# Kernel tuning notes

Measured on AMD Instinct MI355X. Metric: run time of the kernel, lower is better.

The kernel has to match this reference:

```python
import jax, jax.numpy as jnp
import numpy as np

C = 384
K = 13
EPS = 1e-5

def bn(y, g, b, m, v):
    # inference-mode BatchNorm2d over channel dim of NCHW
    scale = (g / jnp.sqrt(v + EPS)).reshape(1, -1, 1, 1)
    shift = (b - m * g / jnp.sqrt(v + EPS)).reshape(1, -1, 1, 1)
    return y * scale + shift

def dwconv(x, w):
    # depthwise KxK conv, SAME padding, w: [C,1,K,K]
    p = w.shape[-1] // 2
    return jax.lax.conv_general_dilated(
        x, w, window_strides=(1, 1), padding=[(p, p), (p, p)],
        dimension_numbers=('NCHW', 'OIHW', 'NCHW'),
        feature_group_count=x.shape[1])

def setup_inputs() -> dict:
    key = jax.random.key(0)
    ks = jax.random.split(key, 16)
    f32 = jnp.float32
    inp = {
        'x':     jax.random.normal(ks[0], (16, C, 56, 56), dtype=f32),
        'pw_w':  jax.random.normal(ks[1], (C, C), dtype=f32) * 0.05,
        'pw_g':  jax.random.uniform(ks[2], (C,), dtype=f32) + 0.5,
        'pw_b':  jax.random.normal(ks[3], (C,), dtype=f32) * 0.1,
        'pw_m':  jax.random.normal(ks[4], (C,), dtype=f32) * 0.1,
        'pw_v':  jax.random.uniform(ks[5], (C,), dtype=f32) + 0.5,
        'dwk_w': jax.random.normal(ks[6], (C, 1, K, K), dtype=f32) * 0.05,
        'dwk_g': jax.random.uniform(ks[7], (C,), dtype=f32) + 0.5,
        'dwk_b': jax.random.normal(ks[8], (C,), dtype=f32) * 0.1,
        'dwk_m': jax.random.normal(ks[9], (C,), dtype=f32) * 0.1,
        'dwk_v': jax.random.uniform(ks[10], (C,), dtype=f32) + 0.5,
        'dw1_w': jax.random.normal(ks[11], (C,), dtype=f32) * 0.5,
        'dw1_g': jax.random.uniform(ks[12], (C,), dtype=f32) + 0.5,
        'dw1_b': jax.random.normal(ks[13], (C,), dtype=f32) * 0.1,
        'dw1_m': jax.random.normal(ks[14], (C,), dtype=f32) * 0.1,
        'dw1_v': jax.random.uniform(ks[15], (C,), dtype=f32) + 0.5,
    }
    return inp

def reference(x, pw_w, pw_g, pw_b, pw_m, pw_v,
              dwk_w, dwk_g, dwk_b, dwk_m, dwk_v,
              dw1_w, dw1_g, dw1_b, dw1_m, dw1_v):
    # pointwise conv (1x1, dense over channels) + BN, residual add
    y = jnp.einsum('bchw,oc->bohw', x, pw_w)
    x_pw = bn(y, pw_g, pw_b, pw_m, pw_v) + x
    # large-kernel depthwise branch
    out = bn(dwconv(x_pw, dwk_w), dwk_g, dwk_b, dwk_m, dwk_v)
    # 1x1 depthwise branch = per-channel scale
    out = out + bn(x_pw * dw1_w.reshape(1, -1, 1, 1), dw1_g, dw1_b, dw1_m, dw1_v)
    return jax.nn.gelu(out, approximate=False)
```

## Files before the change

### kernel.cpp

```cpp
#include <hip/hip_runtime.h>

#define CC 384
#define HW 3136
#define WIDTH 56
#define PLANE_ELEMS (CC*HW)
#define EPS 1e-5f

#define SLOT_U 6272
#define HALF_U 3136

typedef __attribute__((ext_vector_type(8))) short bf16x8;
typedef __attribute__((ext_vector_type(4))) float f32x4;

static __device__ __forceinline__ float bf2f(unsigned short u) {
  union { unsigned int i; float f; } x; x.i = ((unsigned int)u) << 16; return x.f;
}
static __device__ __forceinline__ unsigned short f2bf(float f) {
  union { float f; unsigned int i; } x; x.f = f;
  unsigned int r = x.i + 0x7fffu + ((x.i >> 16) & 1u);
  return (unsigned short)(r >> 16);
}

__global__ __launch_bounds__(256) void pw_gemm_bn_res(
    const float* __restrict__ xin,
    const float* __restrict__ wmat,
    const float* __restrict__ pwg, const float* __restrict__ pwb,
    const float* __restrict__ pwm, const float* __restrict__ pwv,
    unsigned short* __restrict__ xpw)
{
  __shared__ __align__(16) unsigned short Xt[64 * 40];
  __shared__ __align__(16) unsigned short Wt[64 * 40];
  __shared__ float scaleS[64];
  __shared__ float shiftS[64];

  const int tid = threadIdx.x;
  const int j0 = blockIdx.x * 64;
  const int o0 = blockIdx.y * 64;
  const int b  = blockIdx.z;
  const size_t bbase = (size_t)b * PLANE_ELEMS;

  if (tid < 64) {
    int o = o0 + tid;
    float s = pwg[o] * rsqrtf(pwv[o] + EPS);
    scaleS[tid] = s;
    shiftS[tid] = pwb[o] - pwm[o] * s;
  }

  f32x4 acc0 = {0.f,0.f,0.f,0.f}, acc1 = {0.f,0.f,0.f,0.f};
  f32x4 acc2 = {0.f,0.f,0.f,0.f}, acc3 = {0.f,0.f,0.f,0.f};

  const int lane = tid & 63;
  const int wv_  = tid >> 6;
  const int l15  = lane & 15;
  const int q    = lane >> 4;

  const int skk  = tid >> 3;
  const int sjj  = (tid & 7) << 3;
  const int sn   = tid >> 2;
  const int skk0 = (tid & 3) << 3;

  for (int kt = 0; kt < 12; ++kt) {
    const int c0 = kt * 32;
    __syncthreads();
    {
      const float* src = xin + bbase + (size_t)(c0 + skk) * HW + (j0 + sjj);
      float4 p0 = *((const float4*)src);
      float4 p1 = *((const float4*)(src + 4));
      Xt[(sjj + 0) * 40 + skk] = f2bf(p0.x);
      Xt[(sjj + 1) * 40 + skk] = f2bf(p0.y);
      Xt[(sjj + 2) * 40 + skk] = f2bf(p0.z);
      Xt[(sjj + 3) * 40 + skk] = f2bf(p0.w);
      Xt[(sjj + 4) * 40 + skk] = f2bf(p1.x);
      Xt[(sjj + 5) * 40 + skk] = f2bf(p1.y);
      Xt[(sjj + 6) * 40 + skk] = f2bf(p1.z);
      Xt[(sjj + 7) * 40 + skk] = f2bf(p1.w);
    }
    {
      const float* src = wmat + (size_t)(o0 + sn) * CC + (c0 + skk0);
      float4 p0 = *((const float4*)src);
      float4 p1 = *((const float4*)(src + 4));
      ushort4 u0, u1;
      u0.x = f2bf(p0.x); u0.y = f2bf(p0.y); u0.z = f2bf(p0.z); u0.w = f2bf(p0.w);
      u1.x = f2bf(p1.x); u1.y = f2bf(p1.y); u1.z = f2bf(p1.z); u1.w = f2bf(p1.w);
      *((ushort4*)&Wt[sn * 40 + skk0])     = u0;
      *((ushort4*)&Wt[sn * 40 + skk0 + 4]) = u1;
    }
    __syncthreads();

    bf16x8 a  = *((const bf16x8*)&Xt[(wv_ * 16 + l15) * 40 + q * 8]);
    bf16x8 b0 = *((const bf16x8*)&Wt[( 0 + l15) * 40 + q * 8]);
    bf16x8 b1 = *((const bf16x8*)&Wt[(16 + l15) * 40 + q * 8]);
    bf16x8 b2 = *((const bf16x8*)&Wt[(32 + l15) * 40 + q * 8]);
    bf16x8 b3 = *((const bf16x8*)&Wt[(48 + l15) * 40 + q * 8]);
    acc0 = __builtin_amdgcn_mfma_f32_16x16x32_bf16(a, b0, acc0, 0, 0, 0);
    acc1 = __builtin_amdgcn_mfma_f32_16x16x32_bf16(a, b1, acc1, 0, 0, 0);
    acc2 = __builtin_amdgcn_mfma_f32_16x16x32_bf16(a, b2, acc2, 0, 0, 0);
    acc3 = __builtin_amdgcn_mfma_f32_16x16x32_bf16(a, b3, acc3, 0, 0, 0);
  }

  const int j = j0 + wv_ * 16 + q * 4;
  #pragma unroll
  for (int nb = 0; nb < 4; ++nb) {
    f32x4 acc = (nb == 0) ? acc0 : (nb == 1) ? acc1 : (nb == 2) ? acc2 : acc3;
    int oo = nb * 16 + l15;
    int o = o0 + oo;
    float s = scaleS[oo], t = shiftS[oo];
    float4 xr = *((const float4*)(xin + bbase + (size_t)o * HW + j));
    ushort4 w4;
    w4.x = f2bf(acc[0] * s + t + xr.x);
    w4.y = f2bf(acc[1] * s + t + xr.y);
    w4.z = f2bf(acc[2] * s + t + xr.z);
    w4.w = f2bf(acc[3] * s + t + xr.w);
    size_t pidx = (size_t)(b * CC + o) * SLOT_U + HALF_U + j;
    *((ushort4*)(xpw + pidx)) = w4;
  }
}

#define TSTRIDE 88
#define TROWS 76

__global__ __launch_bounds__(256) void dw_conv_mfma(
    float* __restrict__ outf,
    const unsigned short* __restrict__ stash,
    const float* __restrict__ dwkw,
    const float* __restrict__ dkg, const float* __restrict__ dkb,
    const float* __restrict__ dkm, const float* __restrict__ dkv,
    const float* __restrict__ d1w,
    const float* __restrict__ d1g, const float* __restrict__ d1b,
    const float* __restrict__ d1m, const float* __restrict__ d1v)
{
  __shared__ __align__(16) unsigned short tile[TROWS * TSTRIDE];
  __shared__ __align__(16) unsigned short Bt[13 * 16 * 32];

  const int bc = blockIdx.x;
  const int c = bc % CC;
  const size_t plane_u = (size_t)bc * SLOT_U + HALF_U;
  const size_t plane_f = (size_t)bc * HW;
  const int tid = threadIdx.x;

  for (int i = tid; i < TROWS * TSTRIDE; i += 256) {
    int r = i / TSTRIDE, col = i - r * TSTRIDE;
    int gy = r - 6, gx = col - 6;
    unsigned short v = 0;
    if ((unsigned)gy < (unsigned)WIDTH && (unsigned)gx < (unsigned)WIDTH)
      v = stash[plane_u + gy * WIDTH + gx];
    tile[i] = v;
  }
  for (int i = tid; i < 13 * 512; i += 256) {
    int ky = i >> 9, rem = i & 511, n = rem >> 5, k = rem & 31;
    int kx = k - n;
    float wv = ((unsigned)kx < 13u) ? dwkw[c * 169 + ky * 13 + kx] : 0.f;
    Bt[i] = f2bf(wv);
  }

  const float sk = dkg[c] * rsqrtf(dkv[c] + EPS);
  const float tk = dkb[c] - dkm[c] * sk;
  const float s1 = d1g[c] * rsqrtf(d1v[c] + EPS);
  const float a1 = d1w[c] * s1;
  const float t1 = d1b[c] - d1m[c] * s1;
  const float tsum = tk + t1;

  __syncthreads();

  const int lane = tid & 63;
  const int l15  = lane & 15;
  const int q    = lane >> 4;
  const int wid  = tid >> 6;

  bf16x8 bfr[13];
  #pragma unroll
  for (int ky = 0; ky < 13; ++ky)
    bfr[ky] = *((const bf16x8*)&Bt[(ky * 16 + l15) * 32 + q * 8]);

  for (int t = wid; t < 16; t += 4) {
    const int y0 = (t >> 2) * 16, x0 = (t & 3) * 16;
    f32x4 acc = {0.f, 0.f, 0.f, 0.f};
    #pragma unroll
    for (int ky = 0; ky < 13; ++ky) {
      bf16x8 a = *((const bf16x8*)&tile[(y0 + l15 + ky) * TSTRIDE + x0 + q * 8]);
      acc = __builtin_amdgcn_mfma_f32_16x16x32_bf16(a, bfr[ky], acc, 0, 0, 0);
    }
    const int x = x0 + l15;
    if (x < WIDTH) {
      #pragma unroll
      for (int r = 0; r < 4; ++r) {
        const int y = y0 + q * 4 + r;
        if (y < WIDTH) {
          float ctr = bf2f(tile[(y + 6) * TSTRIDE + x + 6]);
          float v = acc[r] * sk + tsum + ctr * a1;
          outf[plane_f + y * WIDTH + x] =
              0.5f * v * (1.f + erff(v * 0.70710678118654752f));
        }
      }
    }
  }
}

extern "C" void kernel_launch(void* const* d_in, const int* in_sizes, int n_in,
                              void* d_out, int out_size, void* d_ws, size_t ws_size,
                              hipStream_t stream) {
  const float* x     = (const float*)d_in[0];
  const float* pw_w  = (const float*)d_in[1];
  const float* pw_g  = (const float*)d_in[2];
  const float* pw_b  = (const float*)d_in[3];
  const float* pw_m  = (const float*)d_in[4];
  const float* pw_v  = (const float*)d_in[5];
  const float* dwk_w = (const float*)d_in[6];
  const float* dwk_g = (const float*)d_in[7];
  const float* dwk_b = (const float*)d_in[8];
  const float* dwk_m = (const float*)d_in[9];
  const float* dwk_v = (const float*)d_in[10];
  const float* dw1_w = (const float*)d_in[11];
  const float* dw1_g = (const float*)d_in[12];
  const float* dw1_b = (const float*)d_in[13];
  const float* dw1_m = (const float*)d_in[14];
  const float* dw1_v = (const float*)d_in[15];
  float* outf = (float*)d_out;
  unsigned short* outu = (unsigned short*)d_out;

  dim3 gridA(HW / 64, CC / 64, 16);
  pw_gemm_bn_res<<<gridA, 256, 0, stream>>>(x, pw_w, pw_g, pw_b, pw_m, pw_v, outu);

  dim3 gridB(16 * CC);
  dw_conv_mfma<<<gridB, 256, 0, stream>>>(outf, outu, dwk_w,
      dwk_g, dwk_b, dwk_m, dwk_v, dw1_w, dw1_g, dw1_b, dw1_m, dw1_v);
}
```

Baseline: 306.6 us.

## Load GEMM operands straight into registers and vectorize depthwise tile fill

The pointwise GEMM kernel no longer stages X and W through LDS with barriers. Each lane loads its MFMA fragments directly from global memory, using strided scalar loads for X and float4 loads for W, and packs them to bf16 with the packed conversion intrinsic. The BN scale and shift are now computed per lane instead of through shared memory. The depthwise kernel fills its halo tile with 16-byte vector loads by shifting the tile origin to an 8-element aligned offset, with the weight band and centre index adjusted to match. The trade is fewer barriers and fewer LDS transposes against uncoalesced strided X loads and redundant W loads across waves.

```diff
diff --git a/kernel.cpp b/kernel.cpp
--- a/kernel.cpp
+++ b/kernel.cpp
@@ -1,4 +1,5 @@
 #include <hip/hip_runtime.h>
+#include <hip/hip_bf16.h>
 
 #define CC 384
 #define HW 3136
@@ -19,6 +20,10 @@
   union { float f; unsigned int i; } x; x.f = f;
   unsigned int r = x.i + 0x7fffu + ((x.i >> 16) & 1u);
   return (unsigned short)(r >> 16);
+}
+static __device__ __forceinline__ unsigned int pkbf(float a, float b) {
+  __hip_bfloat162 h = __float22bfloat162_rn(float2{a, b});
+  union { __hip_bfloat162 h; unsigned int u; } c; c.h = h; return c.u;
 }
 
 __global__ __launch_bounds__(256) void pw_gemm_bn_res(
@@ -28,83 +33,61 @@
     const float* __restrict__ pwm, const float* __restrict__ pwv,
     unsigned short* __restrict__ xpw)
 {
-  __shared__ __align__(16) unsigned short Xt[64 * 40];
-  __shared__ __align__(16) unsigned short Wt[64 * 40];
-  __shared__ float scaleS[64];
-  __shared__ float shiftS[64];
-
   const int tid = threadIdx.x;
   const int j0 = blockIdx.x * 64;
   const int o0 = blockIdx.y * 64;
   const int b  = blockIdx.z;
   const size_t bbase = (size_t)b * PLANE_ELEMS;
 
-  if (tid < 64) {
-    int o = o0 + tid;
-    float s = pwg[o] * rsqrtf(pwv[o] + EPS);
-    scaleS[tid] = s;
-    shiftS[tid] = pwb[o] - pwm[o] * s;
-  }
-
-  f32x4 acc0 = {0.f,0.f,0.f,0.f}, acc1 = {0.f,0.f,0.f,0.f};
-  f32x4 acc2 = {0.f,0.f,0.f,0.f}, acc3 = {0.f,0.f,0.f,0.f};
-
   const int lane = tid & 63;
   const int wv_  = tid >> 6;
   const int l15  = lane & 15;
   const int q    = lane >> 4;
 
-  const int skk  = tid >> 3;
-  const int sjj  = (tid & 7) << 3;
-  const int sn   = tid >> 2;
-  const int skk0 = (tid & 3) << 3;
+  const int jm = j0 + wv_ * 16 + l15;
+  const float* xcol = xin + bbase + jm;
+
+  f32x4 acc0 = {0.f,0.f,0.f,0.f}, acc1 = {0.f,0.f,0.f,0.f};
+  f32x4 acc2 = {0.f,0.f,0.f,0.f}, acc3 = {0.f,0.f,0.f,0.f};
 
   for (int kt = 0; kt < 12; ++kt) {
-    const int c0 = kt * 32;
-    __syncthreads();
-    {
-      const float* src = xin + bbase + (size_t)(c0 + skk) * HW + (j0 + sjj);
-      float4 p0 = *((const float4*)src);
-      float4 p1 = *((const float4*)(src + 4));
-      Xt[(sjj + 0) * 40 + skk] = f2bf(p0.x);
-      Xt[(sjj + 1) * 40 + skk] = f2bf(p0.y);
-      Xt[(sjj + 2) * 40 + skk] = f2bf(p0.z);
-      Xt[(sjj + 3) * 40 + skk] = f2bf(p0.w);
-      Xt[(sjj + 4) * 40 + skk] = f2bf(p1.x);
-      Xt[(sjj + 5) * 40 + skk] = f2bf(p1.y);
-      Xt[(sjj + 6) * 40 + skk] = f2bf(p1.z);
-      Xt[(sjj + 7) * 40 + skk] = f2bf(p1.w);
+    const int c0 = kt * 32 + q * 8;
+    const float* xp = xcol + (size_t)c0 * HW;
+    float a0 = xp[0];
+    float a1 = xp[(size_t)1 * HW];
+    float a2 = xp[(size_t)2 * HW];
+    float a3 = xp[(size_t)3 * HW];
+    float a4 = xp[(size_t)4 * HW];
+    float a5 = xp[(size_t)5 * HW];
+    float a6 = xp[(size_t)6 * HW];
+    float a7 = xp[(size_t)7 * HW];
+    union { bf16x8 v; unsigned int u[4]; } A;
+    A.u[0] = pkbf(a0, a1); A.u[1] = pkbf(a2, a3);
+    A.u[2] = pkbf(a4, a5); A.u[3] = pkbf(a6, a7);
+
+    const float* wrow = wmat + c0 + (size_t)(o0 + l15) * CC;
+    #pragma unroll
+    for (int nb = 0; nb < 4; ++nb) {
+      const float* wp = wrow + (size_t)(nb * 16) * CC;
+      float4 w0 = *((const float4*)wp);
+      float4 w1 = *((const float4*)(wp + 4));
+      union { bf16x8 v; unsigned int u[4]; } B;
+      B.u[0] = pkbf(w0.x, w0.y); B.u[1] = pkbf(w0.z, w0.w);
+      B.u[2] = pkbf(w1.x, w1.y); B.u[3] = pkbf(w1.z, w1.w);
+      if (nb == 0) acc0 = __builtin_amdgcn_mfma_f32_16x16x32_bf16(A.v, B.v, acc0, 0, 0, 0);
+      if (nb == 1) acc1 = __builtin_amdgcn_mfma_f32_16x16x32_bf16(A.v, B.v, acc1, 0, 0, 0);
+      if (nb == 2) acc2 = __builtin_amdgcn_mfma_f32_16x16x32_bf16(A.v, B.v, acc2, 0, 0, 0);
+      if (nb == 3) acc3 = __builtin_amdgcn_mfma_f32_16x16x32_bf16(A.v, B.v, acc3, 0, 0, 0);
     }
-    {
-      const float* src = wmat + (size_t)(o0 + sn) * CC + (c0 + skk0);
-      float4 p0 = *((const float4*)src);
-      float4 p1 = *((const float4*)(src + 4));
-      ushort4 u0, u1;
-      u0.x = f2bf(p0.x); u0.y = f2bf(p0.y); u0.z = f2bf(p0.z); u0.w = f2bf(p0.w);
-      u1.x = f2bf(p1.x); u1.y = f2bf(p1.y); u1.z = f2bf(p1.z); u1.w = f2bf(p1.w);
-      *((ushort4*)&Wt[sn * 40 + skk0])     = u0;
-      *((ushort4*)&Wt[sn * 40 + skk0 + 4]) = u1;
-    }
-    __syncthreads();
-
-    bf16x8 a  = *((const bf16x8*)&Xt[(wv_ * 16 + l15) * 40 + q * 8]);
-    bf16x8 b0 = *((const bf16x8*)&Wt[( 0 + l15) * 40 + q * 8]);
-    bf16x8 b1 = *((const bf16x8*)&Wt[(16 + l15) * 40 + q * 8]);
-    bf16x8 b2 = *((const bf16x8*)&Wt[(32 + l15) * 40 + q * 8]);
-    bf16x8 b3 = *((const bf16x8*)&Wt[(48 + l15) * 40 + q * 8]);
-    acc0 = __builtin_amdgcn_mfma_f32_16x16x32_bf16(a, b0, acc0, 0, 0, 0);
-    acc1 = __builtin_amdgcn_mfma_f32_16x16x32_bf16(a, b1, acc1, 0, 0, 0);
-    acc2 = __builtin_amdgcn_mfma_f32_16x16x32_bf16(a, b2, acc2, 0, 0, 0);
-    acc3 = __builtin_amdgcn_mfma_f32_16x16x32_bf16(a, b3, acc3, 0, 0, 0);
   }
 
   const int j = j0 + wv_ * 16 + q * 4;
   #pragma unroll
   for (int nb = 0; nb < 4; ++nb) {
     f32x4 acc = (nb == 0) ? acc0 : (nb == 1) ? acc1 : (nb == 2) ? acc2 : acc3;
-    int oo = nb * 16 + l15;
-    int o = o0 + oo;
-    float s = scaleS[oo], t = shiftS[oo];
+    int o = o0 + nb * 16 + l15;
+    float s = pwg[o] * rsqrtf(pwv[o] + EPS);
+    float t = pwb[o] - pwm[o] * s;
     float4 xr = *((const float4*)(xin + bbase + (size_t)o * HW + j));
     ushort4 w4;
     w4.x = f2bf(acc[0] * s + t + xr.x);
@@ -138,17 +121,16 @@
   const size_t plane_f = (size_t)bc * HW;
   const int tid = threadIdx.x;
 
-  for (int i = tid; i < TROWS * TSTRIDE; i += 256) {
-    int r = i / TSTRIDE, col = i - r * TSTRIDE;
-    int gy = r - 6, gx = col - 6;
-    unsigned short v = 0;
-    if ((unsigned)gy < (unsigned)WIDTH && (unsigned)gx < (unsigned)WIDTH)
-      v = stash[plane_u + gy * WIDTH + gx];
-    tile[i] = v;
+  for (int i = tid; i < TROWS * 11; i += 256) {
+    int r = i / 11, ch = i - r * 11;
+    uint4 v = {0u, 0u, 0u, 0u};
+    if (r >= 6 && r < 62 && ch >= 1 && ch <= 7)
+      v = *((const uint4*)(stash + plane_u + (r - 6) * WIDTH + (ch - 1) * 8));
+    *((uint4*)&tile[r * TSTRIDE + ch * 8]) = v;
   }
   for (int i = tid; i < 13 * 512; i += 256) {
     int ky = i >> 9, rem = i & 511, n = rem >> 5, k = rem & 31;
-    int kx = k - n;
+    int kx = k - n - 2;
     float wv = ((unsigned)kx < 13u) ? dwkw[c * 169 + ky * 13 + kx] : 0.f;
     Bt[i] = f2bf(wv);
   }
@@ -186,7 +168,7 @@
       for (int r = 0; r < 4; ++r) {
         const int y = y0 + q * 4 + r;
         if (y < WIDTH) {
-          float ctr = bf2f(tile[(y + 6) * TSTRIDE + x + 6]);
+          float ctr = bf2f(tile[(y + 6) * TSTRIDE + x + 8]);
           float v = acc[r] * sk + tsum + ctr * a1;
           outf[plane_f + y * WIDTH + x] =
               0.5f * v * (1.f + erff(v * 0.70710678118654752f));
```

Result: slower. 426.0 us (+39.0%).
